# Kernel tuning notes

Measured on AMD Instinct MI355X. Metric: run time of the kernel, lower is better.

The kernel has to match this reference:

```python
import jax, jax.numpy as jnp
import numpy as np

RESOLUTION = 7
RATIOS = (0.25, 0.125, 0.0625, 0.03125)  # spatial scales for P2..P5
SAMPLE_RATIO = 2
BASE_SIZE = 224.0
BASE_LEVEL = 4.0
LEVEL_MIN = 2.0  # -log2(1/4)
LEVEL_MAX = 5.0  # -log2(1/32)
EPS = 1e-6
IMG = 800.0


def _make_boxes(key, n):
    k1, k2, k3, k4 = jax.random.split(key, 4)
    # log-uniform box sizes in [16, 512] px so rois hit all FPN levels
    w = jnp.exp2(jax.random.uniform(k1, (n,), minval=4.0, maxval=9.0))
    h = jnp.exp2(jax.random.uniform(k2, (n,), minval=4.0, maxval=9.0))
    cx = jax.random.uniform(k3, (n,), minval=0.0, maxval=IMG)
    cy = jax.random.uniform(k4, (n,), minval=0.0, maxval=IMG)
    x1 = jnp.clip(cx - w / 2, 0.0, IMG - 1)
    y1 = jnp.clip(cy - h / 2, 0.0, IMG - 1)
    x2 = jnp.clip(cx + w / 2, 0.0, IMG - 1)
    y2 = jnp.clip(cy + h / 2, 0.0, IMG - 1)
    return jnp.stack([x1, y1, jnp.maximum(x2, x1), jnp.maximum(y2, y1)], axis=1)


def setup_inputs() -> dict:
    key = jax.random.key(0)
    ks = jax.random.split(key, 8)
    N, C = 2, 256
    sizes = [(200, 200), (100, 100), (50, 50), (25, 25), (13, 13)]
    feats = {f"feat{i}": jax.random.normal(ks[i], (N, C, h, w), dtype=jnp.float32)
             for i, (h, w) in enumerate(sizes)}
    feats["props0"] = _make_boxes(ks[5], 512)
    feats["props1"] = _make_boxes(ks[6], 512)
    return feats


def _axis_interp(v, size):
    """Per-axis bilinear setup, matching torchvision RoIAlign (aligned=False)."""
    valid = (v >= -1.0) & (v <= size)
    v0 = jnp.maximum(v, 0.0)
    lo = jnp.floor(v0).astype(jnp.int32)
    at_edge = lo >= size - 1
    lo = jnp.where(at_edge, size - 1, lo)
    hi = jnp.where(at_edge, size - 1, lo + 1)
    frac = jnp.where(at_edge, 0.0, v0 - lo.astype(v.dtype))
    return lo, hi, frac, valid


def _roi_align(feat, rois, scale, res=RESOLUTION, sr=SAMPLE_RATIO):
    """feat: [N,C,H,W], rois: [R,5] (batch_idx,x1,y1,x2,y2) -> [R,C,res,res]."""
    N, C, H, W = feat.shape
    b = rois[:, 0].astype(jnp.int32)
    x1, y1, x2, y2 = (rois[:, 1] * scale, rois[:, 2] * scale,
                      rois[:, 3] * scale, rois[:, 4] * scale)
    roi_w = jnp.maximum(x2 - x1, 1.0)
    roi_h = jnp.maximum(y2 - y1, 1.0)
    bin_w = roi_w / res
    bin_h = roi_h / res
    P = res * sr
    offs = (jnp.arange(P, dtype=jnp.float32) + 0.5) / sr  # sample offsets in bin units
    ys = y1[:, None] + offs[None, :] * bin_h[:, None]  # [R,P]
    xs = x1[:, None] + offs[None, :] * bin_w[:, None]  # [R,P]
    yl, yh, fy, vy = _axis_interp(ys, H)
    xl, xh, fx, vx = _axis_interp(xs, W)
    bi = b[:, None, None]

    def g(yi, xi):  # gather corner values -> [R,P,P,C]
        return feat[bi, :, yi[:, :, None], xi[:, None, :]]

    hy, hx = 1.0 - fy, 1.0 - fx
    val = (g(yl, xl) * (hy[:, :, None] * hx[:, None, :])[..., None]
           + g(yl, xh) * (hy[:, :, None] * fx[:, None, :])[..., None]
           + g(yh, xl) * (fy[:, :, None] * hx[:, None, :])[..., None]
           + g(yh, xh) * (fy[:, :, None] * fx[:, None, :])[..., None])
    val = jnp.where((vy[:, :, None] & vx[:, None, :])[..., None], val, 0.0)
    R = rois.shape[0]
    pooled = val.reshape(R, res, sr, res, sr, C).mean(axis=(2, 4))  # [R,res,res,C]
    return pooled.transpose(0, 3, 1, 2)


def _pool(features, proposals):
    # convert: concat proposals with batch indices -> rois [R,5]
    inds = jnp.concatenate([jnp.full((p.shape[0], 1), i, dtype=p.dtype)
                            for i, p in enumerate(proposals)], axis=0)
    boxes = jnp.concatenate(proposals, axis=0)
    rois = jnp.concatenate([inds, boxes], axis=1)
    rois = jax.lax.stop_gradient(rois)  # torchvision RoIAlign has no roi grad
    # set_level: FPN level assignment (eq.1 of FPN paper)
    areas = (rois[:, 3] - rois[:, 1] + 1) * (rois[:, 4] - rois[:, 2] + 1)
    sizes = jnp.sqrt(areas)
    levels = jnp.floor(BASE_LEVEL + jnp.log2(sizes / BASE_SIZE + EPS))
    levels = (jnp.clip(levels, LEVEL_MIN, LEVEL_MAX) - LEVEL_MIN).astype(jnp.int32)
    R, C = rois.shape[0], features[0].shape[1]
    results = jnp.zeros((R, C, RESOLUTION, RESOLUTION), dtype=boxes.dtype)
    for lvl in range(len(RATIOS)):  # forward uses features[:-1]
        pooled = _roi_align(features[lvl], rois, RATIOS[lvl])
        results = results + jnp.where((levels == lvl)[:, None, None, None], pooled, 0.0)
    return results


def reference(feat0, feat1, feat2, feat3, feat4, props0, props1):
    return _pool([feat0, feat1, feat2, feat3, feat4], [props0, props1])
```

## Files before the change

kernel.cpp:

```cpp
#include <hip/hip_runtime.h>
#include <math.h>

#define C_CH 256
#define RESO 7
#define NBIN 49

typedef float fx4 __attribute__((ext_vector_type(4)));
typedef unsigned int ux2 __attribute__((ext_vector_type(2)));

__device__ __forceinline__ unsigned short f2bf(float f) {
  unsigned int u = __float_as_uint(f);
  u = (u + 0x7fffu + ((u >> 16) & 1u)) >> 16;
  return (unsigned short)u;
}
__device__ __forceinline__ float bf_lo(unsigned int u) { return __uint_as_float(u << 16); }
__device__ __forceinline__ float bf_hi(unsigned int u) { return __uint_as_float(u & 0xffff0000u); }

struct TArgs {
  const float* src[4];
  unsigned short* dst[4];
  int hw[4];
  int tilesx[4];
  int tbase[5];
  int total;
};

__device__ __forceinline__ void decode_tile(const TArgs& a, int T, int& l, int& hw0,
                                            int& c0, int& n, int& HW) {
  int ll = 0;
  if (T >= a.tbase[1]) ll = 1;
  if (T >= a.tbase[2]) ll = 2;
  if (T >= a.tbase[3]) ll = 3;
  const int idx = T - a.tbase[ll];
  const int txs = a.tilesx[ll];
  const int tx = idx % txs;
  const int rem = idx / txs;
  l = ll;
  hw0 = tx * 64;
  c0 = (rem & 3) * 64;
  n = rem >> 2;
  HW = a.hw[ll];
}

__device__ __forceinline__ void load_tile(const TArgs& a, int l, int hw0, int c0, int n,
                                          int HW, int lane16, int row16, fx4 v[4]) {
  const float* s = a.src[l] + (size_t)n * C_CH * HW;
  if (((HW & 3) == 0) && (hw0 + 64 <= HW)) {
#pragma unroll
    for (int i = 0; i < 4; ++i) {
      const int c_l = row16 + 16 * i;
      v[i] = __builtin_nontemporal_load(
          (const fx4*)(s + (size_t)(c0 + c_l) * HW + hw0 + lane16 * 4));
    }
  } else {
#pragma unroll
    for (int i = 0; i < 4; ++i) {
      const int c_l = row16 + 16 * i;
      const float* row = s + (size_t)(c0 + c_l) * HW;
#pragma unroll
      for (int k = 0; k < 4; ++k) {
        const int hw = hw0 + lane16 * 4 + k;
        v[i][k] = (hw < HW) ? row[hw] : 0.0f;
      }
    }
  }
}

__global__ __launch_bounds__(256) void conv_nhwc_bf16(TArgs a) {
  __shared__ float tile[64][65];
  const int t = threadIdx.x;
  const int lane16 = t & 15;
  const int row16 = t >> 4;
  const int stride = gridDim.x;

  int T = blockIdx.x;
  int l0, hw00, c00, n0, HW0;
  decode_tile(a, T, l0, hw00, c00, n0, HW0);
  fx4 v[4];
  load_tile(a, l0, hw00, c00, n0, HW0, lane16, row16, v);

  while (true) {
    __syncthreads();
#pragma unroll
    for (int i = 0; i < 4; ++i) {
      const int c_l = row16 + 16 * i;
      tile[c_l][lane16 * 4 + 0] = v[i][0];
      tile[c_l][lane16 * 4 + 1] = v[i][1];
      tile[c_l][lane16 * 4 + 2] = v[i][2];
      tile[c_l][lane16 * 4 + 3] = v[i][3];
    }

    const int Tn = T + stride;
    const bool more = Tn < a.total;
    int l1, hw01, c01, n1, HW1;
    fx4 w[4];
    if (more) {
      decode_tile(a, Tn, l1, hw01, c01, n1, HW1);
      load_tile(a, l1, hw01, c01, n1, HW1, lane16, row16, w);
    }
    __syncthreads();

    unsigned short* d = a.dst[l0] + (size_t)n0 * HW0 * C_CH;
#pragma unroll
    for (int i = 0; i < 4; ++i) {
      const int hw_l = row16 + 16 * i;
      const int hww = hw00 + hw_l;
      if (hww < HW0) {
        const int c4 = lane16 * 4;
        ux2 p;
        p.x = (unsigned int)f2bf(tile[c4 + 0][hw_l]) |
              ((unsigned int)f2bf(tile[c4 + 1][hw_l]) << 16);
        p.y = (unsigned int)f2bf(tile[c4 + 2][hw_l]) |
              ((unsigned int)f2bf(tile[c4 + 3][hw_l]) << 16);
        *(ux2*)(d + (size_t)hww * C_CH + c00 + c4) = p;
      }
    }

    if (!more) break;
    T = Tn;
    l0 = l1; hw00 = hw01; c00 = c01; n0 = n1; HW0 = HW1;
#pragma unroll
    for (int i = 0; i < 4; ++i) v[i] = w[i];
  }
}

__global__ __launch_bounds__(512) void roi_gather_bf16(
    const unsigned short* __restrict__ f0, const unsigned short* __restrict__ f1,
    const unsigned short* __restrict__ f2, const unsigned short* __restrict__ f3,
    const float* __restrict__ props0, const float* __restrict__ props1,
    float* __restrict__ out) {
  __shared__ float obuf[NBIN * C_CH];
  __shared__ int s_o0[2][14], s_o1[2][14];
  __shared__ float s_w0[2][14], s_w1[2][14];

  const int r = blockIdx.x;
  const int t = threadIdx.x;
  const int b = (r >= 512) ? 1 : 0;
  const float* pr = (b ? props1 : props0) + (r & 511) * 4;
  const float x1 = pr[0], y1 = pr[1], x2 = pr[2], y2 = pr[3];

  const float size = sqrtf((x2 - x1 + 1.0f) * (y2 - y1 + 1.0f));
  float lv = floorf(4.0f + log2f(size / 224.0f + 1e-6f));
  lv = fminf(fmaxf(lv, 2.0f), 5.0f) - 2.0f;
  const int lvl = (int)lv;

  const int Htab[4] = {200, 100, 50, 25};
  const float stab[4] = {0.25f, 0.125f, 0.0625f, 0.03125f};
  const int H = Htab[lvl];
  const int W = H;
  const float sc = stab[lvl];
  const unsigned short* fl = (lvl == 0) ? f0 : (lvl == 1) ? f1 : (lvl == 2) ? f2 : f3;

  const float rx1 = x1 * sc, ry1 = y1 * sc;
  const float roi_w = fmaxf(x2 * sc - rx1, 1.0f);
  const float roi_h = fmaxf(y2 * sc - ry1, 1.0f);
  const float bw = roi_w / 7.0f, bh = roi_h / 7.0f;

  if (t < 28) {
    const int axis = t / 14;
    const int k = t % 14;
    const float off = ((float)k + 0.5f) * 0.5f;
    const float v = axis ? (rx1 + off * bw) : (ry1 + off * bh);
    const int isz = H;
    const bool valid = (v >= -1.0f) && (v <= (float)isz);
    const float v0 = fmaxf(v, 0.0f);
    int lo = (int)floorf(v0);
    const bool edge = (lo >= isz - 1);
    lo = edge ? isz - 1 : lo;
    const int hi = edge ? isz - 1 : lo + 1;
    const float fr = edge ? 0.0f : (v0 - (float)lo);
    const int mul = axis ? C_CH : W * C_CH;
    s_o0[axis][k] = lo * mul;
    s_o1[axis][k] = hi * mul;
    s_w1[axis][k] = valid ? fr : 0.0f;
    s_w0[axis][k] = valid ? (1.0f - fr) : 0.0f;
  }
  __syncthreads();

  const int wv = t >> 6;
  const int ln = t & 63;
  const int cg = ln & 31;
  const int xt = ln >> 5;
  const size_t HWp = (size_t)H * W;
  const unsigned short* base = fl + (size_t)b * HWp * C_CH + cg * 8;

  for (int bb = wv; bb < NBIN; bb += 8) {
    const int ph = bb / 7, pw = bb - ph * 7;
    float acc[8] = {0.f, 0.f, 0.f, 0.f, 0.f, 0.f, 0.f, 0.f};
#pragma unroll
    for (int s1 = 0; s1 < 2; ++s1) {
      const int sy = 2 * ph + s1;
      const int yo0 = s_o0[0][sy], yo1 = s_o1[0][sy];
      const float wy0 = s_w0[0][sy], wy1 = s_w1[0][sy];
#pragma unroll
      for (int s2 = 0; s2 < 2; ++s2) {
        const int sx = 2 * pw + s2;
        const int xo = xt ? s_o1[1][sx] : s_o0[1][sx];
        const float wx = xt ? s_w1[1][sx] : s_w0[1][sx];
        const uint4 q0 = *(const uint4*)(base + yo0 + xo);
        const uint4 q1 = *(const uint4*)(base + yo1 + xo);
        const float w0 = wx * wy0, w1 = wx * wy1;
        acc[0] += w0 * bf_lo(q0.x) + w1 * bf_lo(q1.x);
        acc[1] += w0 * bf_hi(q0.x) + w1 * bf_hi(q1.x);
        acc[2] += w0 * bf_lo(q0.y) + w1 * bf_lo(q1.y);
        acc[3] += w0 * bf_hi(q0.y) + w1 * bf_hi(q1.y);
        acc[4] += w0 * bf_lo(q0.z) + w1 * bf_lo(q1.z);
        acc[5] += w0 * bf_hi(q0.z) + w1 * bf_hi(q1.z);
        acc[6] += w0 * bf_lo(q0.w) + w1 * bf_lo(q1.w);
        acc[7] += w0 * bf_hi(q0.w) + w1 * bf_hi(q1.w);
      }
    }
#pragma unroll
    for (int k = 0; k < 8; ++k) acc[k] += __shfl_xor(acc[k], 32);
    const int cbase = cg * 8 + xt * 4;
#pragma unroll
    for (int k = 0; k < 4; ++k)
      obuf[(cbase + k) * NBIN + bb] = acc[xt * 4 + k] * 0.25f;
  }
  __syncthreads();

  fx4* o4 = (fx4*)(out + (size_t)r * (NBIN * C_CH));
  const fx4* ob4 = (const fx4*)obuf;
  for (int i = t; i < NBIN * C_CH / 4; i += 512)
    __builtin_nontemporal_store(ob4[i], o4 + i);
}

__global__ __launch_bounds__(256) void roi_gather_nchw(
    const float* __restrict__ f0, const float* __restrict__ f1,
    const float* __restrict__ f2, const float* __restrict__ f3,
    const float* __restrict__ props0, const float* __restrict__ props1,
    float* __restrict__ out) {
  __shared__ float obuf[NBIN * C_CH];
  __shared__ int s_o0[2][14], s_o1[2][14];
  __shared__ float s_w0[2][14], s_w1[2][14];

  const int r = blockIdx.x;
  const int t = threadIdx.x;
  const int b = (r >= 512) ? 1 : 0;
  const float* pr = (b ? props1 : props0) + (r & 511) * 4;
  const float x1 = pr[0], y1 = pr[1], x2 = pr[2], y2 = pr[3];
  const float size = sqrtf((x2 - x1 + 1.0f) * (y2 - y1 + 1.0f));
  float lv = floorf(4.0f + log2f(size / 224.0f + 1e-6f));
  lv = fminf(fmaxf(lv, 2.0f), 5.0f) - 2.0f;
  const int lvl = (int)lv;
  const int Htab[4] = {200, 100, 50, 25};
  const float stab[4] = {0.25f, 0.125f, 0.0625f, 0.03125f};
  const int H = Htab[lvl];
  const int W = H;
  const float sc = stab[lvl];
  const float* fl = (lvl == 0) ? f0 : (lvl == 1) ? f1 : (lvl == 2) ? f2 : f3;
  const float rx1 = x1 * sc, ry1 = y1 * sc;
  const float roi_w = fmaxf(x2 * sc - rx1, 1.0f);
  const float roi_h = fmaxf(y2 * sc - ry1, 1.0f);
  const float bw = roi_w / 7.0f, bh = roi_h / 7.0f;
  if (t < 28) {
    const int axis = t / 14;
    const int k = t % 14;
    const float off = ((float)k + 0.5f) * 0.5f;
    const float v = axis ? (rx1 + off * bw) : (ry1 + off * bh);
    const int isz = H;
    const bool valid = (v >= -1.0f) && (v <= (float)isz);
    const float v0 = fmaxf(v, 0.0f);
    int lo = (int)floorf(v0);
    const bool edge = (lo >= isz - 1);
    lo = edge ? isz - 1 : lo;
    const int hi = edge ? isz - 1 : lo + 1;
    const float fr = edge ? 0.0f : (v0 - (float)lo);
    const int mul = axis ? 1 : W;
    s_o0[axis][k] = lo * mul;
    s_o1[axis][k] = hi * mul;
    s_w1[axis][k] = valid ? fr : 0.0f;
    s_w0[axis][k] = valid ? (1.0f - fr) : 0.0f;
  }
  __syncthreads();
  const int wv = t >> 6;
  const int ln = t & 63;
  const size_t HWp = (size_t)H * W;
  const float* base = fl + ((size_t)b * C_CH + ln * 4) * HWp;
  for (int bb = wv; bb < NBIN; bb += 4) {
    const int ph = bb / 7, pw = bb - ph * 7;
    float4 acc = make_float4(0.f, 0.f, 0.f, 0.f);
    for (int s1 = 0; s1 < 2; ++s1) {
      const int sy = 2 * ph + s1;
      const int yo0 = s_o0[0][sy], yo1 = s_o1[0][sy];
      const float wy0 = s_w0[0][sy], wy1 = s_w1[0][sy];
      for (int s2 = 0; s2 < 2; ++s2) {
        const int sx = 2 * pw + s2;
        const int xo0 = s_o0[1][sx], xo1 = s_o1[1][sx];
        const float w00 = wy0 * s_w0[1][sx], w01 = wy0 * s_w1[1][sx];
        const float w10 = wy1 * s_w0[1][sx], w11 = wy1 * s_w1[1][sx];
        float e[4];
        for (int j = 0; j < 4; ++j) {
          e[j] = w00 * base[j * HWp + yo0 + xo0] + w01 * base[j * HWp + yo0 + xo1] +
                 w10 * base[j * HWp + yo1 + xo0] + w11 * base[j * HWp + yo1 + xo1];
        }
        acc.x += e[0]; acc.y += e[1]; acc.z += e[2]; acc.w += e[3];
      }
    }
    const int c4 = ln * 4;
    obuf[(c4 + 0) * NBIN + bb] = acc.x * 0.25f;
    obuf[(c4 + 1) * NBIN + bb] = acc.y * 0.25f;
    obuf[(c4 + 2) * NBIN + bb] = acc.z * 0.25f;
    obuf[(c4 + 3) * NBIN + bb] = acc.w * 0.25f;
  }
  __syncthreads();
  float4* o4 = (float4*)(out + (size_t)r * (NBIN * C_CH));
  const float4* ob4 = (const float4*)obuf;
  for (int i = t; i < NBIN * C_CH / 4; i += 256) o4[i] = ob4[i];
}

extern "C" void kernel_launch(void* const* d_in, const int* in_sizes, int n_in,
                              void* d_out, int out_size, void* d_ws, size_t ws_size,
                              hipStream_t stream) {
  const float* f0 = (const float*)d_in[0];
  const float* f1 = (const float*)d_in[1];
  const float* f2 = (const float*)d_in[2];
  const float* f3 = (const float*)d_in[3];
  const float* p0 = (const float*)d_in[5];
  const float* p1 = (const float*)d_in[6];
  float* out = (float*)d_out;
  unsigned short* ws = (unsigned short*)d_ws;

  const int HWs[4] = {200 * 200, 100 * 100, 50 * 50, 25 * 25};
  size_t off[4];
  size_t acc = 0;
  for (int l = 0; l < 4; ++l) {
    off[l] = acc;
    acc += (size_t)2 * C_CH * HWs[l];
  }
  const size_t need_bytes = acc * sizeof(unsigned short);

  if (ws_size >= need_bytes) {
    TArgs a;
    a.src[0] = f0; a.src[1] = f1; a.src[2] = f2; a.src[3] = f3;
    int cum = 0;
    for (int l = 0; l < 4; ++l) {
      a.dst[l] = ws + off[l];
      a.hw[l] = HWs[l];
      a.tilesx[l] = (HWs[l] + 63) / 64;
      a.tbase[l] = cum;
      cum += a.tilesx[l] * 4 * 2;
    }
    a.tbase[4] = cum;
    a.total = cum;
    const int nblocks = (cum < 2048) ? cum : 2048;
    conv_nhwc_bf16<<<nblocks, 256, 0, stream>>>(a);
    roi_gather_bf16<<<1024, 512, 0, stream>>>(a.dst[0], a.dst[1], a.dst[2], a.dst[3],
                                              p0, p1, out);
  } else {
    roi_gather_nchw<<<1024, 256, 0, stream>>>(f0, f1, f2, f3, p0, p1, out);
  }
}
```

Measured before the change: 188.7 us.

## Split each ROI gather across two channel-half blocks with four-way corner lanes

The bf16 gather kernel now launches two blocks per ROI, each covering 128 channels. This halves the shared output buffer, so more blocks fit per CU, and launch bounds request higher occupancy. Within a wave, the four bilinear corners go to separate 16-lane groups, each issuing one 16-byte load, and the results are reduced with two xor shuffles. The 0.25 averaging factor is folded into the y weights. The cost is duplicated ROI setup per block and an extra shuffle stage.

```diff
diff --git a/kernel.cpp b/kernel.cpp
--- a/kernel.cpp
+++ b/kernel.cpp
@@ -4,6 +4,7 @@
 #define C_CH 256
 #define RESO 7
 #define NBIN 49
+#define CHALF 128
 
 typedef float fx4 __attribute__((ext_vector_type(4)));
 typedef unsigned int ux2 __attribute__((ext_vector_type(2)));
@@ -124,16 +125,18 @@
   }
 }
 
-__global__ __launch_bounds__(512) void roi_gather_bf16(
+__global__ __launch_bounds__(512, 8) void roi_gather_bf16(
     const unsigned short* __restrict__ f0, const unsigned short* __restrict__ f1,
     const unsigned short* __restrict__ f2, const unsigned short* __restrict__ f3,
     const float* __restrict__ props0, const float* __restrict__ props1,
     float* __restrict__ out) {
-  __shared__ float obuf[NBIN * C_CH];
+  __shared__ float obuf[CHALF * NBIN];
   __shared__ int s_o0[2][14], s_o1[2][14];
   __shared__ float s_w0[2][14], s_w1[2][14];
 
-  const int r = blockIdx.x;
+  const int bid = blockIdx.x;
+  const int r = bid >> 1;
+  const int p = bid & 1;
   const int t = threadIdx.x;
   const int b = (r >= 512) ? 1 : 0;
   const float* pr = (b ? props1 : props0) + (r & 511) * 4;
@@ -170,19 +173,22 @@
     const int hi = edge ? isz - 1 : lo + 1;
     const float fr = edge ? 0.0f : (v0 - (float)lo);
     const int mul = axis ? C_CH : W * C_CH;
+    const float wsc = axis ? 1.0f : 0.25f;
     s_o0[axis][k] = lo * mul;
     s_o1[axis][k] = hi * mul;
-    s_w1[axis][k] = valid ? fr : 0.0f;
-    s_w0[axis][k] = valid ? (1.0f - fr) : 0.0f;
+    s_w1[axis][k] = valid ? fr * wsc : 0.0f;
+    s_w0[axis][k] = valid ? (1.0f - fr) * wsc : 0.0f;
   }
   __syncthreads();
 
   const int wv = t >> 6;
   const int ln = t & 63;
-  const int cg = ln & 31;
-  const int xt = ln >> 5;
+  const int cg = ln & 15;
+  const int sub = ln >> 4;
+  const int xt = sub & 1;
+  const int yt = sub >> 1;
   const size_t HWp = (size_t)H * W;
-  const unsigned short* base = fl + (size_t)b * HWp * C_CH + cg * 8;
+  const unsigned short* base = fl + (size_t)b * HWp * C_CH + p * CHALF + cg * 8;
 
   for (int bb = wv; bb < NBIN; bb += 8) {
     const int ph = bb / 7, pw = bb - ph * 7;
@@ -190,38 +196,39 @@
 #pragma unroll
     for (int s1 = 0; s1 < 2; ++s1) {
       const int sy = 2 * ph + s1;
-      const int yo0 = s_o0[0][sy], yo1 = s_o1[0][sy];
-      const float wy0 = s_w0[0][sy], wy1 = s_w1[0][sy];
+      const int yo = yt ? s_o1[0][sy] : s_o0[0][sy];
+      const float wy = yt ? s_w1[0][sy] : s_w0[0][sy];
 #pragma unroll
       for (int s2 = 0; s2 < 2; ++s2) {
         const int sx = 2 * pw + s2;
         const int xo = xt ? s_o1[1][sx] : s_o0[1][sx];
         const float wx = xt ? s_w1[1][sx] : s_w0[1][sx];
-        const uint4 q0 = *(const uint4*)(base + yo0 + xo);
-        const uint4 q1 = *(const uint4*)(base + yo1 + xo);
-        const float w0 = wx * wy0, w1 = wx * wy1;
-        acc[0] += w0 * bf_lo(q0.x) + w1 * bf_lo(q1.x);
-        acc[1] += w0 * bf_hi(q0.x) + w1 * bf_hi(q1.x);
-        acc[2] += w0 * bf_lo(q0.y) + w1 * bf_lo(q1.y);
-        acc[3] += w0 * bf_hi(q0.y) + w1 * bf_hi(q1.y);
-        acc[4] += w0 * bf_lo(q0.z) + w1 * bf_lo(q1.z);
-        acc[5] += w0 * bf_hi(q0.z) + w1 * bf_hi(q1.z);
-        acc[6] += w0 * bf_lo(q0.w) + w1 * bf_lo(q1.w);
-        acc[7] += w0 * bf_hi(q0.w) + w1 * bf_hi(q1.w);
+        const uint4 q = *(const uint4*)(base + yo + xo);
+        const float w = wy * wx;
+        acc[0] = fmaf(bf_lo(q.x), w, acc[0]);
+        acc[1] = fmaf(bf_hi(q.x), w, acc[1]);
+        acc[2] = fmaf(bf_lo(q.y), w, acc[2]);
+        acc[3] = fmaf(bf_hi(q.y), w, acc[3]);
+        acc[4] = fmaf(bf_lo(q.z), w, acc[4]);
+        acc[5] = fmaf(bf_hi(q.z), w, acc[5]);
+        acc[6] = fmaf(bf_lo(q.w), w, acc[6]);
+        acc[7] = fmaf(bf_hi(q.w), w, acc[7]);
       }
     }
 #pragma unroll
-    for (int k = 0; k < 8; ++k) acc[k] += __shfl_xor(acc[k], 32);
-    const int cbase = cg * 8 + xt * 4;
-#pragma unroll
-    for (int k = 0; k < 4; ++k)
-      obuf[(cbase + k) * NBIN + bb] = acc[xt * 4 + k] * 0.25f;
+    for (int k = 0; k < 8; ++k) {
+      acc[k] += __shfl_xor(acc[k], 16);
+      acc[k] += __shfl_xor(acc[k], 32);
+    }
+    const int c0 = cg * 8 + sub * 2;
+    obuf[(c0 + 0) * NBIN + bb] = acc[sub * 2 + 0];
+    obuf[(c0 + 1) * NBIN + bb] = acc[sub * 2 + 1];
   }
   __syncthreads();
 
-  fx4* o4 = (fx4*)(out + (size_t)r * (NBIN * C_CH));
+  fx4* o4 = (fx4*)(out + (size_t)r * (NBIN * C_CH) + (size_t)p * (CHALF * NBIN));
   const fx4* ob4 = (const fx4*)obuf;
-  for (int i = t; i < NBIN * C_CH / 4; i += 512)
+  for (int i = t; i < CHALF * NBIN / 4; i += 512)
     __builtin_nontemporal_store(ob4[i], o4 + i);
 }
 
@@ -345,7 +352,7 @@
     a.total = cum;
     const int nblocks = (cum < 2048) ? cum : 2048;
     conv_nhwc_bf16<<<nblocks, 256, 0, stream>>>(a);
-    roi_gather_bf16<<<1024, 512, 0, stream>>>(a.dst[0], a.dst[1], a.dst[2], a.dst[3],
+    roi_gather_bf16<<<2048, 512, 0, stream>>>(a.dst[0], a.dst[1], a.dst[2], a.dst[3],
                                               p0, p1, out);
   } else {
     roi_gather_nchw<<<1024, 256, 0, stream>>>(f0, f1, f2, f3, p0, p1, out);
```

Measured after the change: 189.2 us. Within noise of the previous version (+0.3%).
